# Performance work log

Hardware: AMD Instinct MI355X
Metric: run time of the kernel (lower is better)

Reference implementation:

```python
import jax, jax.numpy as jnp
import numpy as np

D_MODEL = 1024
N_HEAD = 16
HEAD_DIM = D_MODEL // N_HEAD


def setup_inputs() -> dict:
    key = jax.random.key(0)
    k1, k2, k3 = jax.random.split(key, 3)
    x = jax.random.normal(k1, (2, 2048, D_MODEL), dtype=jnp.float32)
    w_qkv = jax.random.normal(k2, (D_MODEL, 3 * D_MODEL), dtype=jnp.float32) * (1.0 / np.sqrt(D_MODEL))
    w_proj = jax.random.normal(k3, (D_MODEL, D_MODEL), dtype=jnp.float32) * (1.0 / np.sqrt(D_MODEL))
    return {"x": x, "w_qkv": w_qkv, "w_proj": w_proj}


def reference(x, w_qkv, w_proj):
    bs, sl, dm = x.shape
    qkv = x @ w_qkv                                   # [B,S,3*D]
    qkv = qkv.reshape(bs, sl, 3, N_HEAD, HEAD_DIM)
    q, k, v = qkv[:, :, 0], qkv[:, :, 1], qkv[:, :, 2]  # [B,S,H,d]
    q = q.transpose(0, 2, 1, 3)                        # [B,H,S,d]
    k = k.transpose(0, 2, 1, 3)
    v = v.transpose(0, 2, 1, 3)
    sc = 1.0 / np.sqrt(HEAD_DIM).astype(np.float32)
    attn = jnp.einsum('bhqd,bhkd->bhqk', q, k) * sc    # [B,H,S,S]
    causal = jnp.tril(jnp.ones((sl, sl), dtype=bool))  # True = keep
    attn = jnp.where(causal, attn, -jnp.inf)
    w = jax.nn.softmax(attn, axis=-1)                  # [B,H,S,S] (dropout p=0)
    o = jnp.einsum('bhqk,bhkd->bhqd', w, v)            # [B,H,S,d]
    out = o.transpose(0, 2, 1, 3).reshape(bs, sl, dm)
    out = out @ w_proj
    return (out, w)
```

## Files before the change

kernel.cpp:

```cpp
#include <hip/hip_runtime.h>

typedef _Float16 half8 __attribute__((ext_vector_type(8)));
typedef _Float16 half4 __attribute__((ext_vector_type(4)));
typedef float f32x4 __attribute__((ext_vector_type(4)));

__device__ __forceinline__ void gl2lds16(const _Float16* g, _Float16* l) {
  __builtin_amdgcn_global_load_lds((const __attribute__((address_space(1))) void*)g,
                                   (__attribute__((address_space(3))) void*)l, 16, 0, 0);
}

__device__ __forceinline__ void nt_store4(float* p, f32x4 v) {
  __builtin_nontemporal_store(v, (f32x4*)p);
}

#define PSW(row, col) ((col) ^ (((row) & 7) << 3))

__global__ __launch_bounds__(256) void cvt_kernel(const float* __restrict__ in,
                                                  _Float16* __restrict__ out, int n) {
  int i = (blockIdx.x * 256 + threadIdx.x) * 8;
  if (i >= n) return;
  float4 a = *(const float4*)(in + i);
  float4 b = *(const float4*)(in + i + 4);
  half8 o;
  o[0] = (_Float16)a.x; o[1] = (_Float16)a.y; o[2] = (_Float16)a.z; o[3] = (_Float16)a.w;
  o[4] = (_Float16)b.x; o[5] = (_Float16)b.y; o[6] = (_Float16)b.z; o[7] = (_Float16)b.w;
  *(half8*)(out + i) = o;
}

__global__ __launch_bounds__(256) void cvtT_kernel(const float* __restrict__ in,
                                                   _Float16* __restrict__ out,
                                                   int K, int N) {
  __shared__ float Ts[64][65];
  const int k0 = blockIdx.y * 64, n0 = blockIdx.x * 64;
  const int t = threadIdx.x;
  const int r = t >> 4, c = (t & 15) * 4;
#pragma unroll
  for (int i = 0; i < 4; i++) {
    float4 v = *(const float4*)(in + (size_t)(k0 + r + i * 16) * N + n0 + c);
    Ts[r + i * 16][c] = v.x; Ts[r + i * 16][c + 1] = v.y;
    Ts[r + i * 16][c + 2] = v.z; Ts[r + i * 16][c + 3] = v.w;
  }
  __syncthreads();
  const int nl = t >> 2, kq = (t & 3) * 16;
  half8 o0, o1;
#pragma unroll
  for (int j = 0; j < 8; j++) {
    o0[j] = (_Float16)Ts[kq + j][nl];
    o1[j] = (_Float16)Ts[kq + 8 + j][nl];
  }
  *(half8*)(out + (size_t)(n0 + nl) * K + k0 + kq) = o0;
  *(half8*)(out + (size_t)(n0 + nl) * K + k0 + kq + 8) = o1;
}

__global__ __launch_bounds__(256) void vtrans_kernel(const _Float16* __restrict__ v,
                                                     _Float16* __restrict__ vt) {
  __shared__ _Float16 Ht[64][72];
  const int s0 = blockIdx.x * 64;
  const _Float16* vb = v + (size_t)blockIdx.y * 131072;
  _Float16* vtb = vt + (size_t)blockIdx.y * 131072;
  const int t = threadIdx.x;
  const int sl = t >> 3, dq = (t & 7) * 8;
  *(half8*)&Ht[sl][dq] = *(const half8*)(vb + (s0 + sl) * 64 + dq);
  *(half8*)&Ht[sl + 32][dq] = *(const half8*)(vb + (s0 + sl + 32) * 64 + dq);
  __syncthreads();
  const int dl = t >> 2, sq = (t & 3) * 16;
  half8 o0, o1;
#pragma unroll
  for (int j = 0; j < 8; j++) {
    o0[j] = Ht[sq + j][dl];
    o1[j] = Ht[sq + 8 + j][dl];
  }
  *(half8*)(vtb + (size_t)dl * 2048 + s0 + sq) = o0;
  *(half8*)(vtb + (size_t)dl * 2048 + s0 + sq + 8) = o1;
}

template <int MODE, int BN>
__global__ __launch_bounds__(256) void gemm16(const _Float16* __restrict__ A,
                                              const _Float16* __restrict__ B,
                                              float* __restrict__ Cf,
                                              _Float16* __restrict__ Ch,
                                              int M, int N, int K) {
  constexpr int MI = (BN == 128) ? 4 : 2;
  __shared__ __align__(16) _Float16 As[128 * 32];
  __shared__ __align__(16) _Float16 Bs[BN * 32];
  const int tid = threadIdx.x;
  const int lane = tid & 63;
  const int wid = tid >> 6;
  const int quad = lane >> 4;
  const int l16 = lane & 15;
  const int mbase = (BN == 128) ? (wid >> 1) * 64 : wid * 32;
  const int nbase = (BN == 128) ? (wid & 1) * 64 : 0;
  const int m0 = blockIdx.y * 128;
  const int n0 = blockIdx.x * BN;

  f32x4 acc[MI][4];
  const f32x4 fz = {0.f, 0.f, 0.f, 0.f};
#pragma unroll
  for (int i = 0; i < MI; i++)
#pragma unroll
    for (int j = 0; j < 4; j++) acc[i][j] = fz;

  const int srow = tid >> 2;
  const int kq = (tid & 3) * 8;

  for (int kt = 0; kt < K; kt += 32) {
    gl2lds16(A + (size_t)(m0 + srow) * K + kt + kq, &As[tid * 8]);
    gl2lds16(A + (size_t)(m0 + 64 + srow) * K + kt + kq, &As[2048 + tid * 8]);
    gl2lds16(B + (size_t)(n0 + srow) * K + kt + kq, &Bs[tid * 8]);
    if (BN == 128)
      gl2lds16(B + (size_t)(n0 + 64 + srow) * K + kt + kq, &Bs[2048 + tid * 8]);
    __syncthreads();
    half8 af[MI], bf[4];
#pragma unroll
    for (int mi = 0; mi < MI; mi++)
      af[mi] = *(const half8*)&As[(mbase + mi * 16 + l16) * 32 + quad * 8];
#pragma unroll
    for (int ni = 0; ni < 4; ni++)
      bf[ni] = *(const half8*)&Bs[(nbase + ni * 16 + l16) * 32 + quad * 8];
#pragma unroll
    for (int mi = 0; mi < MI; mi++)
#pragma unroll
      for (int ni = 0; ni < 4; ni++)
        acc[mi][ni] = __builtin_amdgcn_mfma_f32_16x16x32_f16(af[mi], bf[ni], acc[mi][ni], 0, 0, 0);
    __syncthreads();
  }

#pragma unroll
  for (int mi = 0; mi < MI; mi++)
#pragma unroll
    for (int ni = 0; ni < 4; ni++)
#pragma unroll
      for (int r = 0; r < 4; r++) {
        int row = m0 + mbase + mi * 16 + quad * 4 + r;
        int col = n0 + nbase + ni * 16 + l16;
        float v = acc[mi][ni][r];
        if (MODE == 0) {
          Cf[(size_t)row * N + col] = v;
        } else {
          int which = col >> 10, h = (col >> 6) & 15, d = col & 63;
          int b = row >> 11, s = row & 2047;
          if (which == 0) v *= 0.125f;
          Ch[((((size_t)(which * 2 + b) * 16 + h) * 2048) + s) * 64 + d] = (_Float16)v;
        }
      }
}

__global__ __launch_bounds__(256) void attn_kernel(const _Float16* __restrict__ qkv,
                                                   const _Float16* __restrict__ vt,
                                                   float* __restrict__ w_out,
                                                   _Float16* __restrict__ o_buf) {
  const int qt = 31 - blockIdx.x;
  const int bh = blockIdx.y;
  const int tid = threadIdx.x;
  const int lane = tid & 63;
  const int wid = tid >> 6;
  const int quad = lane >> 4;
  const int l16 = lane & 15;

  const _Float16* qp = qkv + (size_t)bh * 131072;
  const _Float16* kp = qp + 4194304;
  const _Float16* vtb = vt + (size_t)bh * 131072;

  __shared__ __align__(16) _Float16 Ks[2][4096];
  __shared__ __align__(16) _Float16 Vs[2][4096];
  __shared__ __align__(16) _Float16 Ps[64][64];

  const int qrow = qt * 64 + wid * 16 + l16;
  const half8 qa0 = *(const half8*)(qp + qrow * 64 + quad * 8);
  const half8 qa1 = *(const half8*)(qp + qrow * 64 + 32 + quad * 8);

  const int srow = tid >> 2;
  const int blk8 = (tid & 3) * 8;
  const f32x4 fz = {0.f, 0.f, 0.f, 0.f};
  const int qloc = wid * 16 + l16;
  const int kbase = quad * 4;

  float* wbase = w_out + (size_t)bh * 4194304 + (size_t)qt * 131072;

  {
    const int rr = tid >> 4, cc = (tid & 15) * 4;
    for (int kt = qt + 1; kt < 32; kt++) {
      float* wz = wbase + (size_t)kt * 64 + cc;
#pragma unroll
      for (int p = 0; p < 4; p++)
        nt_store4(wz + (size_t)(p * 16 + rr) * 2048, fz);
    }
  }

  float lsum = 0.f;

  int cur = 0;
  gl2lds16(kp + (size_t)srow * 64 + blk8, &Ks[0][tid * 8]);
  gl2lds16(kp + (size_t)srow * 64 + 32 + blk8, &Ks[0][2048 + tid * 8]);
  __syncthreads();
  for (int kt = 0; kt <= qt; kt++) {
    if (kt < qt) {
      gl2lds16(kp + (size_t)((kt + 1) * 64 + srow) * 64 + blk8, &Ks[cur ^ 1][tid * 8]);
      gl2lds16(kp + (size_t)((kt + 1) * 64 + srow) * 64 + 32 + blk8, &Ks[cur ^ 1][2048 + tid * 8]);
    }
    f32x4 sacc[4];
    __builtin_amdgcn_s_setprio(1);
#pragma unroll
    for (int ni = 0; ni < 4; ni++) {
      half8 kb0 = *(const half8*)&Ks[cur][(ni * 16 + l16) * 32 + quad * 8];
      half8 kb1 = *(const half8*)&Ks[cur][2048 + (ni * 16 + l16) * 32 + quad * 8];
      f32x4 s = fz;
      s = __builtin_amdgcn_mfma_f32_16x16x32_f16(kb0, qa0, s, 0, 0, 0);
      s = __builtin_amdgcn_mfma_f32_16x16x32_f16(kb1, qa1, s, 0, 0, 0);
      sacc[ni] = s;
    }
    __builtin_amdgcn_s_setprio(0);
    if (kt < qt) {
#pragma unroll
      for (int ni = 0; ni < 4; ni++)
#pragma unroll
        for (int r = 0; r < 4; r++) lsum += __expf(sacc[ni][r]);
    } else {
#pragma unroll
      for (int ni = 0; ni < 4; ni++)
#pragma unroll
        for (int r = 0; r < 4; r++) {
          if (ni * 16 + kbase + r <= qloc) lsum += __expf(sacc[ni][r]);
        }
    }
    __syncthreads();
    cur ^= 1;
  }
  lsum += __shfl_xor(lsum, 16);
  lsum += __shfl_xor(lsum, 32);
  const float invl = 1.0f / lsum;

  f32x4 oacc[4];
#pragma unroll
  for (int di = 0; di < 4; di++) oacc[di] = fz;

  cur = 0;
  gl2lds16(kp + (size_t)srow * 64 + blk8, &Ks[0][tid * 8]);
  gl2lds16(kp + (size_t)srow * 64 + 32 + blk8, &Ks[0][2048 + tid * 8]);
  gl2lds16(vtb + (size_t)srow * 2048 + blk8, &Vs[0][tid * 8]);
  gl2lds16(vtb + (size_t)srow * 2048 + 32 + blk8, &Vs[0][2048 + tid * 8]);
  __syncthreads();
  for (int kt = 0; kt <= qt; kt++) {
    if (kt > 0) {
      const int erow = lane >> 2;
      const int ec = (lane & 3) * 4;
      const _Float16* prow = &Ps[wid * 16 + erow][0];
      float* wrow = wbase + (size_t)(wid * 16 + erow) * 2048 + (kt - 1) * 64;
#pragma unroll
      for (int j = 0; j < 4; j++) {
        half4 h = *(const half4*)(prow + PSW(erow, j * 16 + ec));
        f32x4 o;
        o[0] = (float)h[0]; o[1] = (float)h[1]; o[2] = (float)h[2]; o[3] = (float)h[3];
        nt_store4(wrow + j * 16 + ec, o);
      }
    }
    if (kt < qt) {
      const int kn = kt + 1;
      gl2lds16(kp + (size_t)(kn * 64 + srow) * 64 + blk8, &Ks[cur ^ 1][tid * 8]);
      gl2lds16(kp + (size_t)(kn * 64 + srow) * 64 + 32 + blk8, &Ks[cur ^ 1][2048 + tid * 8]);
      gl2lds16(vtb + (size_t)srow * 2048 + kn * 64 + blk8, &Vs[cur ^ 1][tid * 8]);
      gl2lds16(vtb + (size_t)srow * 2048 + kn * 64 + 32 + blk8, &Vs[cur ^ 1][2048 + tid * 8]);
    }
    f32x4 sacc[4];
    __builtin_amdgcn_s_setprio(1);
#pragma unroll
    for (int ni = 0; ni < 4; ni++) {
      half8 kb0 = *(const half8*)&Ks[cur][(ni * 16 + l16) * 32 + quad * 8];
      half8 kb1 = *(const half8*)&Ks[cur][2048 + (ni * 16 + l16) * 32 + quad * 8];
      f32x4 s = fz;
      s = __builtin_amdgcn_mfma_f32_16x16x32_f16(kb0, qa0, s, 0, 0, 0);
      s = __builtin_amdgcn_mfma_f32_16x16x32_f16(kb1, qa1, s, 0, 0, 0);
      sacc[ni] = s;
    }
    __builtin_amdgcn_s_setprio(0);
    const bool diag = (kt == qt);
#pragma unroll
    for (int ni = 0; ni < 4; ni++) {
      half4 ph;
#pragma unroll
      for (int r = 0; r < 4; r++) {
        float p = __expf(sacc[ni][r]) * invl;
        if (diag && (ni * 16 + kbase + r > qloc)) p = 0.0f;
        ph[r] = (_Float16)p;
      }
      *(half4*)&Ps[qloc][PSW(qloc, ni * 16 + kbase)] = ph;
    }
    __builtin_amdgcn_s_setprio(1);
#pragma unroll
    for (int kk = 0; kk < 2; kk++) {
      half8 pa = *(const half8*)&Ps[wid * 16 + l16][PSW(l16, kk * 32 + quad * 8)];
#pragma unroll
      for (int di = 0; di < 4; di++) {
        half8 vb = *(const half8*)&Vs[cur][kk * 2048 + (di * 16 + l16) * 32 + quad * 8];
        oacc[di] = __builtin_amdgcn_mfma_f32_16x16x32_f16(pa, vb, oacc[di], 0, 0, 0);
      }
    }
    __builtin_amdgcn_s_setprio(0);
    __syncthreads();
    cur ^= 1;
  }
  {
    const int erow = lane >> 2;
    const int ec = (lane & 3) * 4;
    const _Float16* prow = &Ps[wid * 16 + erow][0];
    float* wrow = wbase + (size_t)(wid * 16 + erow) * 2048 + (size_t)qt * 64;
#pragma unroll
    for (int j = 0; j < 4; j++) {
      half4 h = *(const half4*)(prow + PSW(erow, j * 16 + ec));
      f32x4 o;
      o[0] = (float)h[0]; o[1] = (float)h[1]; o[2] = (float)h[2]; o[3] = (float)h[3];
      nt_store4(wrow + j * 16 + ec, o);
    }
  }

  const int b = bh >> 4, h = bh & 15;
#pragma unroll
  for (int di = 0; di < 4; di++)
#pragma unroll
    for (int r = 0; r < 4; r++) {
      int s = qt * 64 + wid * 16 + quad * 4 + r;
      int d = di * 16 + l16;
      o_buf[((size_t)(b * 2048 + s) * 16 + h) * 64 + d] = (_Float16)oacc[di][r];
    }
}

extern "C" void kernel_launch(void* const* d_in, const int* in_sizes, int n_in,
                              void* d_out, int out_size, void* d_ws, size_t ws_size,
                              hipStream_t stream) {
  const float* x = (const float*)d_in[0];
  const float* w_qkv = (const float*)d_in[1];
  const float* w_proj = (const float*)d_in[2];
  float* out = (float*)d_out;
  float* w_attn = out + (size_t)4194304;

  char* ws = (char*)d_ws;
  _Float16* x16 = (_Float16*)ws;
  _Float16* wqkvT = (_Float16*)(ws + (size_t)(8 << 20));
  _Float16* wprojT = (_Float16*)(ws + (size_t)(14 << 20));
  _Float16* qkvb = (_Float16*)(ws + (size_t)(16 << 20));
  _Float16* vT = (_Float16*)(ws + (size_t)(40 << 20));
  _Float16* ob = (_Float16*)(ws + (size_t)(48 << 20));

  cvt_kernel<<<2048, 256, 0, stream>>>(x, x16, 4194304);
  cvtT_kernel<<<dim3(48, 16), 256, 0, stream>>>(w_qkv, wqkvT, 1024, 3072);
  cvtT_kernel<<<dim3(16, 16), 256, 0, stream>>>(w_proj, wprojT, 1024, 1024);

  gemm16<1, 128><<<dim3(24, 32), 256, 0, stream>>>(x16, wqkvT, nullptr, qkvb, 4096, 3072, 1024);
  vtrans_kernel<<<dim3(32, 32), 256, 0, stream>>>(qkvb + (size_t)2 * 4194304, vT);
  attn_kernel<<<dim3(32, 32), 256, 0, stream>>>(qkvb, vT, w_attn, ob);
  gemm16<0, 64><<<dim3(16, 32), 256, 0, stream>>>(ob, wprojT, out, nullptr, 4096, 1024, 1024);
}
```

Measured before the change: 687.5 us.

## Replace QKV GEMM with 256x256-tile double-buffered 512-thread kernel

Adds a dedicated QKV projection GEMM that uses 256x256 output tiles, 512 threads, and K=64 stages. Stages are double-buffered in LDS through direct global-to-LDS loads, with the next stage's load overlapping the current MFMA work. The epilogue writes directly into the head-split q/k/v layout and applies the 1/8 scale to q. The goal is more data reuse per tile and overlap of memory with compute. The cost is 128KB of LDS per block and only 192 blocks, which may underfill the GPU's CUs, and the scattered fp16 epilogue stores are not coalesced.

```diff
diff --git a/kernel.cpp b/kernel.cpp
--- a/kernel.cpp
+++ b/kernel.cpp
@@ -72,6 +72,107 @@
   }
   *(half8*)(vtb + (size_t)dl * 2048 + s0 + sq) = o0;
   *(half8*)(vtb + (size_t)dl * 2048 + s0 + sq + 8) = o1;
+}
+
+__global__ __launch_bounds__(512, 2) void gemmqkv(const _Float16* __restrict__ A,
+                                                  const _Float16* __restrict__ B,
+                                                  _Float16* __restrict__ Ch) {
+  __shared__ __align__(16) _Float16 Abuf[2][256 * 64];
+  __shared__ __align__(16) _Float16 Bbuf[2][256 * 64];
+  const int tid = threadIdx.x;
+  const int lane = tid & 63;
+  const int wid = tid >> 6;
+  const int quad = lane >> 4;
+  const int l16 = lane & 15;
+  const int wm = wid >> 2;
+  const int wn = wid & 3;
+  const int m0 = blockIdx.y * 256;
+  const int n0 = blockIdx.x * 256;
+
+  f32x4 acc[8][4];
+  const f32x4 fz = {0.f, 0.f, 0.f, 0.f};
+#pragma unroll
+  for (int i = 0; i < 8; i++)
+#pragma unroll
+    for (int j = 0; j < 4; j++) acc[i][j] = fz;
+
+  int srow[4], scol[4], sdst[4];
+#pragma unroll
+  for (int j = 0; j < 4; j++) {
+    int p = (j * 512 + tid) * 16;
+    int r = p >> 7;
+    int ch = ((p & 127) >> 1) ^ ((r & 7) << 3);
+    srow[j] = r;
+    scol[j] = ch;
+    sdst[j] = p >> 1;
+  }
+
+#define STAGE(kt, s)                                                              \
+  {                                                                               \
+    const int k0_ = (kt) * 64;                                                    \
+    _Float16* as_ = Abuf[s];                                                      \
+    _Float16* bs_ = Bbuf[s];                                                      \
+    _Pragma("unroll")                                                             \
+    for (int j = 0; j < 4; j++)                                                   \
+      gl2lds16(A + (size_t)(m0 + srow[j]) * 1024 + k0_ + scol[j], as_ + sdst[j]); \
+    _Pragma("unroll")                                                             \
+    for (int j = 0; j < 4; j++)                                                   \
+      gl2lds16(B + (size_t)(n0 + srow[j]) * 1024 + k0_ + scol[j], bs_ + sdst[j]); \
+  }
+
+  STAGE(0, 0);
+  for (int t = 0; t < 16; t++) {
+    asm volatile("" ::: "memory");
+    __builtin_amdgcn_s_barrier();
+    asm volatile("" ::: "memory");
+    if (t + 1 < 16) {
+      STAGE(t + 1, (t + 1) & 1);
+      asm volatile("s_waitcnt vmcnt(8)" ::: "memory");
+    } else {
+      asm volatile("s_waitcnt vmcnt(0)" ::: "memory");
+    }
+    __builtin_amdgcn_s_barrier();
+    asm volatile("" ::: "memory");
+
+    const _Float16* Ab = Abuf[t & 1];
+    const _Float16* Bb = Bbuf[t & 1];
+    half8 bf[2][4];
+#pragma unroll
+    for (int kk = 0; kk < 2; kk++)
+#pragma unroll
+      for (int ni = 0; ni < 4; ni++) {
+        int r = wn * 64 + ni * 16 + l16;
+        int c = kk * 32 + quad * 8;
+        bf[kk][ni] = *(const half8*)(Bb + r * 64 + (c ^ ((r & 7) << 3)));
+      }
+#pragma unroll
+    for (int mi = 0; mi < 8; mi++) {
+      int r = wm * 128 + mi * 16 + l16;
+      half8 a0 = *(const half8*)(Ab + r * 64 + ((quad * 8) ^ ((r & 7) << 3)));
+      half8 a1 = *(const half8*)(Ab + r * 64 + ((32 + quad * 8) ^ ((r & 7) << 3)));
+#pragma unroll
+      for (int ni = 0; ni < 4; ni++) {
+        acc[mi][ni] = __builtin_amdgcn_mfma_f32_16x16x32_f16(a0, bf[0][ni], acc[mi][ni], 0, 0, 0);
+        acc[mi][ni] = __builtin_amdgcn_mfma_f32_16x16x32_f16(a1, bf[1][ni], acc[mi][ni], 0, 0, 0);
+      }
+    }
+  }
+#undef STAGE
+
+#pragma unroll
+  for (int mi = 0; mi < 8; mi++)
+#pragma unroll
+    for (int ni = 0; ni < 4; ni++)
+#pragma unroll
+      for (int r = 0; r < 4; r++) {
+        int row = m0 + wm * 128 + mi * 16 + quad * 4 + r;
+        int col = n0 + wn * 64 + ni * 16 + l16;
+        float v = acc[mi][ni][r];
+        int which = col >> 10, h = (col >> 6) & 15, d = col & 63;
+        int b = row >> 11, s = row & 2047;
+        if (which == 0) v *= 0.125f;
+        Ch[((((size_t)(which * 2 + b) * 16 + h) * 2048) + s) * 64 + d] = (_Float16)v;
+      }
 }
 
 template <int MODE, int BN>
@@ -345,7 +446,7 @@
   cvtT_kernel<<<dim3(48, 16), 256, 0, stream>>>(w_qkv, wqkvT, 1024, 3072);
   cvtT_kernel<<<dim3(16, 16), 256, 0, stream>>>(w_proj, wprojT, 1024, 1024);
 
-  gemm16<1, 128><<<dim3(24, 32), 256, 0, stream>>>(x16, wqkvT, nullptr, qkvb, 4096, 3072, 1024);
+  gemmqkv<<<dim3(12, 16), 512, 0, stream>>>(x16, wqkvT, qkvb);
   vtrans_kernel<<<dim3(32, 32), 256, 0, stream>>>(qkvb + (size_t)2 * 4194304, vT);
   attn_kernel<<<dim3(32, 32), 256, 0, stream>>>(qkvb, vT, w_attn, ob);
   gemm16<0, 64><<<dim3(16, 32), 256, 0, stream>>>(ob, wprojT, out, nullptr, 4096, 1024, 1024);
```

After: 683.2 us. No clear change (-0.6%).
